# Optimization experiments

Hardware: AMD Instinct MI355X
Metric: run time of the kernel (lower is better)

The kernel has to match this reference:

```python
import jax, jax.numpy as jnp
import numpy as np

N_NODES = 50000
N_EDGES = 800000
D_FEAT = 128
DIM = 3
IN_CH = DIM + 2 * D_FEAT  # 259
HID = 256
OUT = 128


def setup_inputs() -> dict:
    key = jax.random.key(0)
    ks = jax.random.split(key, 10)
    x = jax.random.normal(ks[0], (N_NODES, D_FEAT), dtype=jnp.float32)
    pos = jax.random.normal(ks[1], (N_NODES, DIM), dtype=jnp.float32)
    edge_index = jax.random.randint(ks[2], (2, N_EDGES), 0, N_NODES, dtype=jnp.int64)
    s0 = 1.0 / np.sqrt(IN_CH)
    s2 = 1.0 / np.sqrt(HID)
    W0 = jax.random.uniform(ks[3], (HID, IN_CH), jnp.float32, -s0, s0)
    b0 = jax.random.uniform(ks[4], (HID,), jnp.float32, -s0, s0)
    W2 = jax.random.uniform(ks[5], (HID, HID), jnp.float32, -s2, s2)
    b2 = jax.random.uniform(ks[6], (HID,), jnp.float32, -s2, s2)
    W3 = jax.random.uniform(ks[7], (OUT, HID), jnp.float32, -s2, s2)
    b3 = jax.random.uniform(ks[8], (OUT,), jnp.float32, -s2, s2)
    return {"x": x, "edge_index": edge_index, "pos": pos,
            "W0": W0, "b0": b0, "W2": W2, "b2": b2, "W3": W3, "b3": b3}


def reference(x, edge_index, pos, W0, b0, W2, b2, W3, b3):
    src, dst = edge_index[0], edge_index[1]
    edge_attr = pos[dst] - pos[src]              # [E, 3]
    node_i = x[src]                              # [E, D]
    node_j = x[dst]                              # [E, D]
    inp = jnp.concatenate((edge_attr, node_i, node_j), axis=1)  # [E, 259]
    h = jax.nn.elu(inp @ W0.T + b0)
    h = jax.nn.elu(h @ W2.T + b2)
    return h @ W3.T + b3                         # [E, 128]
```

## Files before the change

kernel.cpp:

```cpp
#include <hip/hip_runtime.h>
#include <cstddef>
#include <cstdint>


#define N_NODES_C 50000
#define N_EDGES_C 800000
#define D_FEAT_C  128
#define IN_CH_C   259
#define HID_C     256
#define OUT_CH_C  128

#define BM6    64
#define HSTR6  264

typedef unsigned short u16;
typedef short bf16x8 __attribute__((ext_vector_type(8)));
typedef float f32x4 __attribute__((ext_vector_type(4)));

__device__ __forceinline__ u16 f2bf(float f) {
    union { float f; unsigned u; } v; v.f = f;
    unsigned u = v.u;
    return (u16)((u + 0x7fffu + ((u >> 16) & 1u)) >> 16);
}
__device__ __forceinline__ unsigned cvt_pk_bf16(float lo, float hi) {
    unsigned r;
    asm("v_cvt_pk_bf16_f32 %0, %1, %2" : "=v"(r) : "v"(lo), "v"(hi));
    return r;
}
__device__ __forceinline__ float bf2f_lo(unsigned u) {
    union { unsigned u; float f; } v; v.u = u << 16; return v.f;
}
__device__ __forceinline__ float bf2f_hi(unsigned u) {
    union { unsigned u; float f; } v; v.u = u & 0xFFFF0000u; return v.f;
}
__device__ __forceinline__ float elu1(float x) {
    return x > 0.0f ? x : (__expf(x) - 1.0f);
}
__device__ __forceinline__ unsigned addelu_pk(unsigned a, unsigned b) {
    float s0 = elu1(bf2f_lo(a) + bf2f_lo(b));
    float s1 = elu1(bf2f_hi(a) + bf2f_hi(b));
    return cvt_pk_bf16(s0, s1);
}

__global__ void detect_idx64(const void* __restrict__ ei_raw, int* __restrict__ flag) {
    if (blockIdx.x == 0 && threadIdx.x == 0) {
        const unsigned long long* p = (const unsigned long long*)ei_raw;
        int is64 = 1;
        for (int i = 0; i < 64; ++i)
            if (p[i] >= (1ULL << 32)) { is64 = 0; break; }
        *flag = is64;
    }
}

__global__ void prep_weights(const float* __restrict__ W0, const float* __restrict__ W2,
                             const float* __restrict__ W3, u16* __restrict__ WAB,
                             u16* __restrict__ W2f, u16* __restrict__ W3f) {
    int i = blockIdx.x * blockDim.x + threadIdx.x;
    const int nwab = 512 * 160, nw2 = 256 * 256, nw3 = 128 * 256;
    if (i < nwab) {
        int j = i / 160, k = i - j * 160;
        float v = 0.f;
        if (j < 256) {
            if (k < 128) v = W0[j * IN_CH_C + 3 + k];
            else if (k < 131) v = -W0[j * IN_CH_C + (k - 128)];
        } else {
            int j2 = j - 256;
            if (k < 128) v = W0[j2 * IN_CH_C + 131 + k];
            else if (k < 131) v = W0[j2 * IN_CH_C + (k - 128)];
        }
        WAB[i] = f2bf(v);
    } else if (i < nwab + nw2) {
        int q = i - nwab;
        int c = q & 7, lIdx = (q >> 3) & 63, kk = (q >> 9) & 7, jb = q >> 12;
        int j = jb * 16 + (lIdx & 15);
        int k = kk * 32 + ((lIdx >> 4) << 3) + c;
        W2f[q] = f2bf(W2[j * 256 + k]);
    } else if (i < nwab + nw2 + nw3) {
        int q = i - nwab - nw2;
        int c = q & 7, lIdx = (q >> 3) & 63, kk = (q >> 9) & 7, ob = q >> 12;
        int o = ob * 16 + (lIdx & 15);
        int k = kk * 32 + ((lIdx >> 4) << 3) + c;
        W3f[q] = f2bf(W3[o * 256 + k]);
    }
}

extern "C" __global__ void __launch_bounds__(512, 2)
node_gemm(const float* __restrict__ x, const float* __restrict__ pos,
          const u16* __restrict__ WAB, const float* __restrict__ b0,
          u16* __restrict__ AB) {
    __shared__ u16 tile[128 * 168];
    const int t = threadIdx.x;
    const int row0 = blockIdx.x * 128;
    for (int idx = t; idx < 128 * 80; idx += 512) {
        int m = idx / 80, wq = idx - m * 80;
        int k = wq * 2, n = row0 + m;
        float f0 = 0.f, f1 = 0.f;
        if (n < N_NODES_C) {
            f0 = (k < 128) ? x[(size_t)n * 128 + k] : (k < 131 ? pos[(size_t)n * 3 + k - 128] : 0.f);
            int k1 = k + 1;
            f1 = (k1 < 128) ? x[(size_t)n * 128 + k1] : (k1 < 131 ? pos[(size_t)n * 3 + k1 - 128] : 0.f);
        }
        *(unsigned*)&tile[m * 168 + k] = (unsigned)f2bf(f0) | ((unsigned)f2bf(f1) << 16);
    }
    __syncthreads();
    const int w = t >> 6, l = t & 63, lr = l & 15, hi = l >> 4;
    for (int mc = 0; mc < 2; ++mc) {
        f32x4 acc[4][4];
#pragma unroll
        for (int ji = 0; ji < 4; ++ji)
#pragma unroll
            for (int mi = 0; mi < 4; ++mi)
                acc[ji][mi] = (f32x4){0.f, 0.f, 0.f, 0.f};
#pragma unroll
        for (int kk = 0; kk < 5; ++kk) {
            bf16x8 af[4], bfr[4];
#pragma unroll
            for (int ji = 0; ji < 4; ++ji)
                af[ji] = *(const bf16x8*)&WAB[(size_t)(w * 64 + ji * 16 + lr) * 160 + kk * 32 + hi * 8];
#pragma unroll
            for (int mi = 0; mi < 4; ++mi)
                bfr[mi] = *(const bf16x8*)&tile[(mc * 64 + mi * 16 + lr) * 168 + kk * 32 + hi * 8];
#pragma unroll
            for (int ji = 0; ji < 4; ++ji)
#pragma unroll
                for (int mi = 0; mi < 4; ++mi)
                    acc[ji][mi] = __builtin_amdgcn_mfma_f32_16x16x32_bf16(af[ji], bfr[mi], acc[ji][mi], 0, 0, 0);
        }
#pragma unroll
        for (int ji = 0; ji < 4; ++ji) {
            int j0 = w * 64 + ji * 16 + hi * 4;
            float4 bb = make_float4(0.f, 0.f, 0.f, 0.f);
            if (j0 < 256) bb = *(const float4*)&b0[j0];
#pragma unroll
            for (int mi = 0; mi < 4; ++mi) {
                int nn = row0 + mc * 64 + mi * 16 + lr;
                if (nn < N_NODES_C) {
                    f32x4 v = acc[ji][mi];
                    uint2 pr;
                    pr.x = cvt_pk_bf16(v[0] + bb.x, v[1] + bb.y);
                    pr.y = cvt_pk_bf16(v[2] + bb.z, v[3] + bb.w);
                    *(uint2*)&AB[(size_t)nn * 512 + j0] = pr;
                }
            }
        }
    }
}

extern "C" __global__ void __launch_bounds__(256, 4)
edge_mlp_v6(const u16* __restrict__ AB, const void* __restrict__ ei_raw,
            const int* __restrict__ idx64_flag,
            const u16* __restrict__ W2f, const float* __restrict__ b2,
            const u16* __restrict__ W3f, const float* __restrict__ b3,
            float* __restrict__ out) {
    __shared__ u16 hbuf[BM6 * HSTR6];

    const int t = threadIdx.x;
    const int e0 = blockIdx.x * BM6;
    const int w = t >> 6, l = t & 63, lr = l & 15, hi = l >> 4;

    {
        const int m = t >> 2, q0 = (t & 3) * 2;
        const int eid = e0 + m;
        int sA, sB;
        if (*idx64_flag) {
            const long long* e = (const long long*)ei_raw;
            sA = (int)e[eid]; sB = (int)e[N_EDGES_C + eid];
        } else {
            const int* e = (const int*)ei_raw;
            sA = e[eid]; sB = e[N_EDGES_C + eid];
        }
        const u16* ra = AB + (size_t)sA * 512 + q0 * 32;
        const u16* rb = AB + (size_t)sB * 512 + 256 + q0 * 32;
        uint4 a[8], b[8];
#pragma unroll
        for (int i = 0; i < 8; ++i) a[i] = *(const uint4*)(ra + i * 8);
#pragma unroll
        for (int i = 0; i < 8; ++i) b[i] = *(const uint4*)(rb + i * 8);
#pragma unroll
        for (int i = 0; i < 8; ++i) {
            uint4 r;
            r.x = addelu_pk(a[i].x, b[i].x);
            r.y = addelu_pk(a[i].y, b[i].y);
            r.z = addelu_pk(a[i].z, b[i].z);
            r.w = addelu_pk(a[i].w, b[i].w);
            *(uint4*)&hbuf[m * HSTR6 + q0 * 32 + i * 8] = r;
        }
    }
    __syncthreads();

    f32x4 acc[4][4];
#pragma unroll
    for (int ji = 0; ji < 4; ++ji) {
        const float4 bb = *(const float4*)&b2[w * 64 + ji * 16 + hi * 4];
#pragma unroll
        for (int mi = 0; mi < 4; ++mi)
            acc[ji][mi] = (f32x4){bb.x, bb.y, bb.z, bb.w};
    }
    __builtin_amdgcn_s_setprio(1);
#pragma unroll
    for (int kk = 0; kk < 8; ++kk) {
        bf16x8 af[4], bfr[4];
#pragma unroll
        for (int ji = 0; ji < 4; ++ji)
            af[ji] = *(const bf16x8*)&W2f[(size_t)(((w * 4 + ji) * 8 + kk) * 64 + l) * 8];
#pragma unroll
        for (int mi = 0; mi < 4; ++mi)
            bfr[mi] = *(const bf16x8*)&hbuf[(mi * 16 + lr) * HSTR6 + kk * 32 + hi * 8];
#pragma unroll
        for (int ji = 0; ji < 4; ++ji)
#pragma unroll
            for (int mi = 0; mi < 4; ++mi)
                acc[ji][mi] = __builtin_amdgcn_mfma_f32_16x16x32_bf16(af[ji], bfr[mi], acc[ji][mi], 0, 0, 0);
    }
    __builtin_amdgcn_s_setprio(0);
    __syncthreads();

#pragma unroll
    for (int ji = 0; ji < 4; ++ji) {
        int j0 = w * 64 + ji * 16 + hi * 4;
#pragma unroll
        for (int mi = 0; mi < 4; ++mi) {
            int mm = mi * 16 + lr;
            f32x4 v = acc[ji][mi];
            uint2 pr;
            pr.x = cvt_pk_bf16(elu1(v[0]), elu1(v[1]));
            pr.y = cvt_pk_bf16(elu1(v[2]), elu1(v[3]));
            *(uint2*)&hbuf[mm * HSTR6 + j0] = pr;
        }
    }
    __syncthreads();

    f32x4 acc2[2][4];
#pragma unroll
    for (int oi = 0; oi < 2; ++oi) {
        const float4 bv = *(const float4*)&b3[w * 32 + oi * 16 + hi * 4];
#pragma unroll
        for (int mi = 0; mi < 4; ++mi)
            acc2[oi][mi] = (f32x4){bv.x, bv.y, bv.z, bv.w};
    }
    __builtin_amdgcn_s_setprio(1);
#pragma unroll
    for (int kk = 0; kk < 8; ++kk) {
        bf16x8 af3[2], bh[4];
#pragma unroll
        for (int oi = 0; oi < 2; ++oi)
            af3[oi] = *(const bf16x8*)&W3f[(size_t)(((w * 2 + oi) * 8 + kk) * 64 + l) * 8];
#pragma unroll
        for (int mi = 0; mi < 4; ++mi)
            bh[mi] = *(const bf16x8*)&hbuf[(mi * 16 + lr) * HSTR6 + kk * 32 + hi * 8];
#pragma unroll
        for (int oi = 0; oi < 2; ++oi)
#pragma unroll
            for (int mi = 0; mi < 4; ++mi)
                acc2[oi][mi] = __builtin_amdgcn_mfma_f32_16x16x32_bf16(af3[oi], bh[mi], acc2[oi][mi], 0, 0, 0);
    }
    __builtin_amdgcn_s_setprio(0);

#pragma unroll
    for (int oi = 0; oi < 2; ++oi)
#pragma unroll
        for (int mi = 0; mi < 4; ++mi) {
            f32x4 v = acc2[oi][mi];
            float4 o4;
            o4.x = v[0]; o4.y = v[1]; o4.z = v[2]; o4.w = v[3];
            *(float4*)&out[(size_t)(e0 + mi * 16 + lr) * 128
                           + w * 32 + oi * 16 + hi * 4] = o4;
        }
}

#define BM 64
#define PAD 65
__global__ void transpose_f32(const float* __restrict__ src, float* __restrict__ dst, int R, int C) {
    int i = blockIdx.x * blockDim.x + threadIdx.x;
    if (i < R * C) { int c = i / R; int r = i - c * R; dst[i] = src[r * C + c]; }
}
__device__ __forceinline__ void layer256(const float* __restrict__ wt, const float* __restrict__ b,
                                         const float* in_lds, float* out_lds, int K, int t) {
    const int jg = t & 63, mc = t >> 6;
    const float* wp = wt + jg * 4;
    const float4 bv = *(const float4*)&b[jg * 4];
    float acc[8][4];
#pragma unroll
    for (int i = 0; i < 8; ++i) { acc[i][0] = bv.x; acc[i][1] = bv.y; acc[i][2] = bv.z; acc[i][3] = bv.w; }
    const float* hbase = in_lds + mc * 8;
    float4 wv = *(const float4*)wp;
    for (int k = 0; k < K; ++k) {
        float4 wn = wv;
        if (k + 1 < K) wn = *(const float4*)(wp + (size_t)(k + 1) * HID_C);
        float h[8];
#pragma unroll
        for (int i = 0; i < 8; ++i) h[i] = hbase[k * PAD + i];
#pragma unroll
        for (int i = 0; i < 8; ++i) {
            acc[i][0] += h[i] * wv.x; acc[i][1] += h[i] * wv.y;
            acc[i][2] += h[i] * wv.z; acc[i][3] += h[i] * wv.w;
        }
        wv = wn;
    }
#pragma unroll
    for (int i4 = 0; i4 < 4; ++i4)
#pragma unroll
        for (int i = 0; i < 8; ++i) {
            float v = acc[i][i4];
            v = v > 0.0f ? v : expm1f(v);
            out_lds[(jg * 4 + i4) * PAD + mc * 8 + i] = v;
        }
}
extern "C" __global__ void __launch_bounds__(512, 2)
edge_mlp_f32(const float* __restrict__ x, const void* __restrict__ ei_raw,
             const float* __restrict__ pos, const int* __restrict__ idx64_flag,
             const float* __restrict__ wt0, const float* __restrict__ b0,
             const float* __restrict__ wt2, const float* __restrict__ b2,
             const float* __restrict__ wt3, const float* __restrict__ b3,
             float* __restrict__ out) {
    __shared__ float buf1[IN_CH_C * PAD];
    __shared__ float buf2[HID_C * PAD];
    __shared__ int s_src[BM], s_dst[BM];
    const int t = threadIdx.x;
    const int e0 = blockIdx.x * BM;
    if (t < BM) {
        int s, d;
        if (*idx64_flag) {
            const long long* e = (const long long*)ei_raw;
            s = (int)e[e0 + t]; d = (int)e[N_EDGES_C + e0 + t];
        } else {
            const int* e = (const int*)ei_raw;
            s = e[e0 + t]; d = e[N_EDGES_C + e0 + t];
        }
        s_src[t] = s; s_dst[t] = d;
    }
    __syncthreads();
    if (t < BM) {
        const int s = s_src[t], d = s_dst[t];
#pragma unroll
        for (int i = 0; i < 3; ++i)
            buf1[i * PAD + t] = pos[d * 3 + i] - pos[s * 3 + i];
    }
    {
        const int l = t & 31, grp = t >> 5;
#pragma unroll
        for (int r = 0; r < 4; ++r) {
            const int m = grp + r * 16;
            const int s = s_src[m], d = s_dst[m];
            const float4 xi = *(const float4*)&x[(size_t)s * D_FEAT_C + l * 4];
            const float4 xj = *(const float4*)&x[(size_t)d * D_FEAT_C + l * 4];
            buf1[(3 + l * 4 + 0) * PAD + m] = xi.x; buf1[(3 + l * 4 + 1) * PAD + m] = xi.y;
            buf1[(3 + l * 4 + 2) * PAD + m] = xi.z; buf1[(3 + l * 4 + 3) * PAD + m] = xi.w;
            buf1[(131 + l * 4 + 0) * PAD + m] = xj.x; buf1[(131 + l * 4 + 1) * PAD + m] = xj.y;
            buf1[(131 + l * 4 + 2) * PAD + m] = xj.z; buf1[(131 + l * 4 + 3) * PAD + m] = xj.w;
        }
    }
    __syncthreads();
    layer256(wt0, b0, buf1, buf2, IN_CH_C, t);
    __syncthreads();
    layer256(wt2, b2, buf2, buf1, HID_C, t);
    __syncthreads();
    {
        const int jg = t & 31, mc = t >> 5;
        const float* wp = wt3 + jg * 4;
        const float4 bv = *(const float4*)&b3[jg * 4];
        float acc[4][4];
#pragma unroll
        for (int i = 0; i < 4; ++i) { acc[i][0] = bv.x; acc[i][1] = bv.y; acc[i][2] = bv.z; acc[i][3] = bv.w; }
        const float* hbase = buf1 + mc * 4;
        float4 wv = *(const float4*)wp;
        for (int k = 0; k < HID_C; ++k) {
            float4 wn = wv;
            if (k + 1 < HID_C) wn = *(const float4*)(wp + (size_t)(k + 1) * OUT_CH_C);
            float h[4];
#pragma unroll
            for (int i = 0; i < 4; ++i) h[i] = hbase[k * PAD + i];
#pragma unroll
            for (int i = 0; i < 4; ++i) {
                acc[i][0] += h[i] * wv.x; acc[i][1] += h[i] * wv.y;
                acc[i][2] += h[i] * wv.z; acc[i][3] += h[i] * wv.w;
            }
            wv = wn;
        }
#pragma unroll
        for (int i = 0; i < 4; ++i) {
            float4 o;
            o.x = acc[i][0]; o.y = acc[i][1]; o.z = acc[i][2]; o.w = acc[i][3];
            *(float4*)&out[(size_t)(e0 + mc * 4 + i) * OUT_CH_C + jg * 4] = o;
        }
    }
}

extern "C" void kernel_launch(void* const* d_in, const int* in_sizes, int n_in,
                              void* d_out, int out_size, void* d_ws, size_t ws_size,
                              hipStream_t stream) {
    const float* x   = (const float*)d_in[0];
    const void*  ei  = d_in[1];
    const float* pos = (const float*)d_in[2];
    const float* W0  = (const float*)d_in[3];
    const float* b0  = (const float*)d_in[4];
    const float* W2  = (const float*)d_in[5];
    const float* b2  = (const float*)d_in[6];
    const float* W3  = (const float*)d_in[7];
    const float* b3  = (const float*)d_in[8];
    float* out = (float*)d_out;

    const size_t need = (size_t)N_NODES_C * 512 * 2 + (size_t)512 * 160 * 2
                      + (size_t)256 * 256 * 2 + (size_t)128 * 256 * 2 + 16;
    if (ws_size >= need) {
        u16* AB  = (u16*)d_ws;
        u16* WAB = AB + (size_t)N_NODES_C * 512;
        u16* W2f = WAB + 512 * 160;
        u16* W3f = W2f + 256 * 256;
        int* flag = (int*)(W3f + 128 * 256);

        detect_idx64<<<1, 64, 0, stream>>>(ei, flag);
        prep_weights<<<704, 256, 0, stream>>>(W0, W2, W3, WAB, W2f, W3f);
        node_gemm<<<391, 512, 0, stream>>>(x, pos, WAB, b0, AB);
        edge_mlp_v6<<<N_EDGES_C / BM6, 256, 0, stream>>>(AB, ei, flag, W2f, b2, W3f, b3, out);
    } else {
        float* wt0 = (float*)d_ws;
        float* wt2 = wt0 + IN_CH_C * HID_C;
        float* wt3 = wt2 + HID_C * HID_C;
        int*   flag = (int*)(wt3 + HID_C * OUT_CH_C);

        detect_idx64<<<1, 64, 0, stream>>>(ei, flag);
        int n0 = HID_C * IN_CH_C;
        transpose_f32<<<(n0 + 255) / 256, 256, 0, stream>>>(W0, wt0, HID_C, IN_CH_C);
        int n2 = HID_C * HID_C;
        transpose_f32<<<(n2 + 255) / 256, 256, 0, stream>>>(W2, wt2, HID_C, HID_C);
        int n3 = OUT_CH_C * HID_C;
        transpose_f32<<<(n3 + 255) / 256, 256, 0, stream>>>(W3, wt3, OUT_CH_C, HID_C);
        edge_mlp_f32<<<N_EDGES_C / BM, 512, 0, stream>>>(
            x, ei, pos, flag, wt0, b0, wt2, b2, wt3, b3, out);
    }
}
```

Measured before the change: 386.1 us.

## Make edge MLP kernel persistent with prefetched gathers and double LDS buffers

Replaces the one-tile-per-block edge MLP with a persistent kernel. A grid of 512 blocks with 512 threads each loops over edge tiles, and the gather of the next tile's node rows is issued before the current tile's GEMMs so that global latency overlaps compute. Two separate LDS buffers hold the layer-1 and layer-2 activations. Barriers wait only on LDS counters, which lets the in-flight global prefetch continue, and the work per wave is halved across eight waves. The trade-off is fewer resident waves per CU and more register pressure from holding the prefetched data across the loop.

```diff
diff --git a/kernel.cpp b/kernel.cpp
--- a/kernel.cpp
+++ b/kernel.cpp
@@ -10,8 +10,10 @@
 #define HID_C     256
 #define OUT_CH_C  128
 
-#define BM6    64
-#define HSTR6  264
+#define BM7    64
+#define NT7    (N_EDGES_C / BM7)
+#define GRID7  512
+#define HSTR7  264
 
 typedef unsigned short u16;
 typedef short bf16x8 __attribute__((ext_vector_type(8)));
@@ -40,6 +42,11 @@
     float s0 = elu1(bf2f_lo(a) + bf2f_lo(b));
     float s1 = elu1(bf2f_hi(a) + bf2f_hi(b));
     return cvt_pk_bf16(s0, s1);
+}
+__device__ __forceinline__ void barrier_lds_only() {
+    asm volatile("s_waitcnt lgkmcnt(0)" ::: "memory");
+    __builtin_amdgcn_s_barrier();
+    __builtin_amdgcn_sched_barrier(0);
 }
 
 __global__ void detect_idx64(const void* __restrict__ ei_raw, int* __restrict__ flag) {
@@ -146,126 +153,124 @@
     }
 }
 
-extern "C" __global__ void __launch_bounds__(256, 4)
-edge_mlp_v6(const u16* __restrict__ AB, const void* __restrict__ ei_raw,
+extern "C" __global__ void __launch_bounds__(512, 4)
+edge_mlp_v7(const u16* __restrict__ AB, const void* __restrict__ ei_raw,
             const int* __restrict__ idx64_flag,
             const u16* __restrict__ W2f, const float* __restrict__ b2,
             const u16* __restrict__ W3f, const float* __restrict__ b3,
             float* __restrict__ out) {
-    __shared__ u16 hbuf[BM6 * HSTR6];
+    __shared__ u16 h1[BM7 * HSTR7];
+    __shared__ u16 h2[BM7 * HSTR7];
 
     const int t = threadIdx.x;
-    const int e0 = blockIdx.x * BM6;
     const int w = t >> 6, l = t & 63, lr = l & 15, hi = l >> 4;
-
-    {
-        const int m = t >> 2, q0 = (t & 3) * 2;
-        const int eid = e0 + m;
-        int sA, sB;
-        if (*idx64_flag) {
-            const long long* e = (const long long*)ei_raw;
-            sA = (int)e[eid]; sB = (int)e[N_EDGES_C + eid];
-        } else {
-            const int* e = (const int*)ei_raw;
-            sA = e[eid]; sB = e[N_EDGES_C + eid];
-        }
-        const u16* ra = AB + (size_t)sA * 512 + q0 * 32;
-        const u16* rb = AB + (size_t)sB * 512 + 256 + q0 * 32;
-        uint4 a[8], b[8];
-#pragma unroll
-        for (int i = 0; i < 8; ++i) a[i] = *(const uint4*)(ra + i * 8);
-#pragma unroll
-        for (int i = 0; i < 8; ++i) b[i] = *(const uint4*)(rb + i * 8);
-#pragma unroll
-        for (int i = 0; i < 8; ++i) {
+    const int m = t >> 3, q = t & 7;
+    const int is64 = *idx64_flag;
+    const long long* e64 = (const long long*)ei_raw;
+    const int* e32 = (const int*)ei_raw;
+
+    float4 bb2[2];
+#pragma unroll
+    for (int ji = 0; ji < 2; ++ji)
+        bb2[ji] = *(const float4*)&b2[w * 32 + ji * 16 + hi * 4];
+    const float4 bb3 = *(const float4*)&b3[w * 16 + hi * 4];
+
+    uint4 ga[4], gb[4];
+#define GATHER(TL) do {                                                         \
+        int eid = (TL) * BM7 + m;                                               \
+        int sA, sB;                                                             \
+        if (is64) { sA = (int)e64[eid]; sB = (int)e64[N_EDGES_C + eid]; }       \
+        else      { sA = e32[eid];      sB = e32[N_EDGES_C + eid]; }            \
+        const u16* ra = AB + (size_t)sA * 512 + q * 32;                         \
+        const u16* rb = AB + (size_t)sB * 512 + 256 + q * 32;                   \
+        _Pragma("unroll")                                                       \
+        for (int i = 0; i < 4; ++i) { ga[i] = *(const uint4*)(ra + i * 8);      \
+                                      gb[i] = *(const uint4*)(rb + i * 8); }    \
+    } while (0)
+
+    const int tile0 = blockIdx.x;
+    GATHER(tile0);
+
+    for (int tk = tile0; tk < NT7; tk += GRID7) {
+#pragma unroll
+        for (int i = 0; i < 4; ++i) {
             uint4 r;
-            r.x = addelu_pk(a[i].x, b[i].x);
-            r.y = addelu_pk(a[i].y, b[i].y);
-            r.z = addelu_pk(a[i].z, b[i].z);
-            r.w = addelu_pk(a[i].w, b[i].w);
-            *(uint4*)&hbuf[m * HSTR6 + q0 * 32 + i * 8] = r;
-        }
-    }
-    __syncthreads();
-
-    f32x4 acc[4][4];
-#pragma unroll
-    for (int ji = 0; ji < 4; ++ji) {
-        const float4 bb = *(const float4*)&b2[w * 64 + ji * 16 + hi * 4];
+            r.x = addelu_pk(ga[i].x, gb[i].x);
+            r.y = addelu_pk(ga[i].y, gb[i].y);
+            r.z = addelu_pk(ga[i].z, gb[i].z);
+            r.w = addelu_pk(ga[i].w, gb[i].w);
+            *(uint4*)&h1[m * HSTR7 + q * 32 + i * 8] = r;
+        }
+        if (tk + GRID7 < NT7) GATHER(tk + GRID7);
+
+        barrier_lds_only();
+
+        f32x4 acc[2][4];
+#pragma unroll
+        for (int ji = 0; ji < 2; ++ji)
+#pragma unroll
+            for (int mi = 0; mi < 4; ++mi)
+                acc[ji][mi] = (f32x4){bb2[ji].x, bb2[ji].y, bb2[ji].z, bb2[ji].w};
+        __builtin_amdgcn_s_setprio(1);
+#pragma unroll
+        for (int kk = 0; kk < 8; ++kk) {
+            bf16x8 af[2], bfr[4];
+#pragma unroll
+            for (int ji = 0; ji < 2; ++ji)
+                af[ji] = *(const bf16x8*)&W2f[(size_t)(((w * 2 + ji) * 8 + kk) * 64 + l) * 8];
+#pragma unroll
+            for (int mi = 0; mi < 4; ++mi)
+                bfr[mi] = *(const bf16x8*)&h1[(mi * 16 + lr) * HSTR7 + kk * 32 + hi * 8];
+#pragma unroll
+            for (int ji = 0; ji < 2; ++ji)
+#pragma unroll
+                for (int mi = 0; mi < 4; ++mi)
+                    acc[ji][mi] = __builtin_amdgcn_mfma_f32_16x16x32_bf16(af[ji], bfr[mi], acc[ji][mi], 0, 0, 0);
+        }
+        __builtin_amdgcn_s_setprio(0);
+
+#pragma unroll
+        for (int ji = 0; ji < 2; ++ji) {
+            int j0 = w * 32 + ji * 16 + hi * 4;
+#pragma unroll
+            for (int mi = 0; mi < 4; ++mi) {
+                int mm = mi * 16 + lr;
+                f32x4 v = acc[ji][mi];
+                uint2 pr;
+                pr.x = cvt_pk_bf16(elu1(v[0]), elu1(v[1]));
+                pr.y = cvt_pk_bf16(elu1(v[2]), elu1(v[3]));
+                *(uint2*)&h2[mm * HSTR7 + j0] = pr;
+            }
+        }
+        barrier_lds_only();
+
+        f32x4 acc2[4];
 #pragma unroll
         for (int mi = 0; mi < 4; ++mi)
-            acc[ji][mi] = (f32x4){bb.x, bb.y, bb.z, bb.w};
-    }
-    __builtin_amdgcn_s_setprio(1);
-#pragma unroll
-    for (int kk = 0; kk < 8; ++kk) {
-        bf16x8 af[4], bfr[4];
-#pragma unroll
-        for (int ji = 0; ji < 4; ++ji)
-            af[ji] = *(const bf16x8*)&W2f[(size_t)(((w * 4 + ji) * 8 + kk) * 64 + l) * 8];
-#pragma unroll
-        for (int mi = 0; mi < 4; ++mi)
-            bfr[mi] = *(const bf16x8*)&hbuf[(mi * 16 + lr) * HSTR6 + kk * 32 + hi * 8];
-#pragma unroll
-        for (int ji = 0; ji < 4; ++ji)
-#pragma unroll
-            for (int mi = 0; mi < 4; ++mi)
-                acc[ji][mi] = __builtin_amdgcn_mfma_f32_16x16x32_bf16(af[ji], bfr[mi], acc[ji][mi], 0, 0, 0);
-    }
-    __builtin_amdgcn_s_setprio(0);
-    __syncthreads();
-
-#pragma unroll
-    for (int ji = 0; ji < 4; ++ji) {
-        int j0 = w * 64 + ji * 16 + hi * 4;
+            acc2[mi] = (f32x4){bb3.x, bb3.y, bb3.z, bb3.w};
+        __builtin_amdgcn_s_setprio(1);
+#pragma unroll
+        for (int kk = 0; kk < 8; ++kk) {
+            bf16x8 af3, bh[4];
+            af3 = *(const bf16x8*)&W3f[(size_t)((w * 8 + kk) * 64 + l) * 8];
+#pragma unroll
+            for (int mi = 0; mi < 4; ++mi)
+                bh[mi] = *(const bf16x8*)&h2[(mi * 16 + lr) * HSTR7 + kk * 32 + hi * 8];
+#pragma unroll
+            for (int mi = 0; mi < 4; ++mi)
+                acc2[mi] = __builtin_amdgcn_mfma_f32_16x16x32_bf16(af3, bh[mi], acc2[mi], 0, 0, 0);
+        }
+        __builtin_amdgcn_s_setprio(0);
+
 #pragma unroll
         for (int mi = 0; mi < 4; ++mi) {
-            int mm = mi * 16 + lr;
-            f32x4 v = acc[ji][mi];
-            uint2 pr;
-            pr.x = cvt_pk_bf16(elu1(v[0]), elu1(v[1]));
-            pr.y = cvt_pk_bf16(elu1(v[2]), elu1(v[3]));
-            *(uint2*)&hbuf[mm * HSTR6 + j0] = pr;
-        }
-    }
-    __syncthreads();
-
-    f32x4 acc2[2][4];
-#pragma unroll
-    for (int oi = 0; oi < 2; ++oi) {
-        const float4 bv = *(const float4*)&b3[w * 32 + oi * 16 + hi * 4];
-#pragma unroll
-        for (int mi = 0; mi < 4; ++mi)
-            acc2[oi][mi] = (f32x4){bv.x, bv.y, bv.z, bv.w};
-    }
-    __builtin_amdgcn_s_setprio(1);
-#pragma unroll
-    for (int kk = 0; kk < 8; ++kk) {
-        bf16x8 af3[2], bh[4];
-#pragma unroll
-        for (int oi = 0; oi < 2; ++oi)
-            af3[oi] = *(const bf16x8*)&W3f[(size_t)(((w * 2 + oi) * 8 + kk) * 64 + l) * 8];
-#pragma unroll
-        for (int mi = 0; mi < 4; ++mi)
-            bh[mi] = *(const bf16x8*)&hbuf[(mi * 16 + lr) * HSTR6 + kk * 32 + hi * 8];
-#pragma unroll
-        for (int oi = 0; oi < 2; ++oi)
-#pragma unroll
-            for (int mi = 0; mi < 4; ++mi)
-                acc2[oi][mi] = __builtin_amdgcn_mfma_f32_16x16x32_bf16(af3[oi], bh[mi], acc2[oi][mi], 0, 0, 0);
-    }
-    __builtin_amdgcn_s_setprio(0);
-
-#pragma unroll
-    for (int oi = 0; oi < 2; ++oi)
-#pragma unroll
-        for (int mi = 0; mi < 4; ++mi) {
-            f32x4 v = acc2[oi][mi];
+            f32x4 v = acc2[mi];
             float4 o4;
             o4.x = v[0]; o4.y = v[1]; o4.z = v[2]; o4.w = v[3];
-            *(float4*)&out[(size_t)(e0 + mi * 16 + lr) * 128
-                           + w * 32 + oi * 16 + hi * 4] = o4;
-        }
+            *(float4*)&out[(size_t)(tk * BM7 + mi * 16 + lr) * 128 + w * 16 + hi * 4] = o4;
+        }
+    }
+#undef GATHER
 }
 
 #define BM 64
@@ -412,7 +417,7 @@
         detect_idx64<<<1, 64, 0, stream>>>(ei, flag);
         prep_weights<<<704, 256, 0, stream>>>(W0, W2, W3, WAB, W2f, W3f);
         node_gemm<<<391, 512, 0, stream>>>(x, pos, WAB, b0, AB);
-        edge_mlp_v6<<<N_EDGES_C / BM6, 256, 0, stream>>>(AB, ei, flag, W2f, b2, W3f, b3, out);
+        edge_mlp_v7<<<GRID7, 512, 0, stream>>>(AB, ei, flag, W2f, b2, W3f, b3, out);
     } else {
         float* wt0 = (float*)d_ws;
         float* wt2 = wt0 + IN_CH_C * HID_C;
```

Result: slower. 511.2 us (+32.4%).

## Split edge MLP over eight waves with swizzled double LDS buffers

Applied to the files above, without the earlier changes.

The edge MLP kernel moves from 256 to 512 threads per 64-edge block. Each wave now computes half as many output columns, so there are more waves to hide latency and fewer accumulators per wave. The gather is spread across more threads, and separate h1/h2 LDS buffers remove one barrier. An XOR swizzle on the LDS columns is meant to reduce bank conflicts, at the cost of doubled shared memory per block, which may limit occupancy.

```diff
diff --git a/kernel.cpp b/kernel.cpp
--- a/kernel.cpp
+++ b/kernel.cpp
@@ -10,8 +10,9 @@
 #define HID_C     256
 #define OUT_CH_C  128
 
-#define BM6    64
-#define HSTR6  264
+#define BM8    64
+#define HSTR8  272
+#define SW(row, c) ((c) ^ (((row) & 7) << 3))
 
 typedef unsigned short u16;
 typedef short bf16x8 __attribute__((ext_vector_type(8)));
@@ -146,20 +147,21 @@
     }
 }
 
-extern "C" __global__ void __launch_bounds__(256, 4)
-edge_mlp_v6(const u16* __restrict__ AB, const void* __restrict__ ei_raw,
+extern "C" __global__ void __launch_bounds__(512, 4)
+edge_mlp_v8(const u16* __restrict__ AB, const void* __restrict__ ei_raw,
             const int* __restrict__ idx64_flag,
             const u16* __restrict__ W2f, const float* __restrict__ b2,
             const u16* __restrict__ W3f, const float* __restrict__ b3,
             float* __restrict__ out) {
-    __shared__ u16 hbuf[BM6 * HSTR6];
+    __shared__ u16 h1[BM8 * HSTR8];
+    __shared__ u16 h2[BM8 * HSTR8];
 
     const int t = threadIdx.x;
-    const int e0 = blockIdx.x * BM6;
+    const int e0 = blockIdx.x * BM8;
     const int w = t >> 6, l = t & 63, lr = l & 15, hi = l >> 4;
 
     {
-        const int m = t >> 2, q0 = (t & 3) * 2;
+        const int m = t >> 3, q = t & 7;
         const int eid = e0 + m;
         int sA, sB;
         if (*idx64_flag) {
@@ -169,29 +171,29 @@
             const int* e = (const int*)ei_raw;
             sA = e[eid]; sB = e[N_EDGES_C + eid];
         }
-        const u16* ra = AB + (size_t)sA * 512 + q0 * 32;
-        const u16* rb = AB + (size_t)sB * 512 + 256 + q0 * 32;
-        uint4 a[8], b[8];
-#pragma unroll
-        for (int i = 0; i < 8; ++i) a[i] = *(const uint4*)(ra + i * 8);
-#pragma unroll
-        for (int i = 0; i < 8; ++i) b[i] = *(const uint4*)(rb + i * 8);
-#pragma unroll
-        for (int i = 0; i < 8; ++i) {
+        const u16* ra = AB + (size_t)sA * 512 + q * 32;
+        const u16* rb = AB + (size_t)sB * 512 + 256 + q * 32;
+        uint4 a[4], b[4];
+#pragma unroll
+        for (int i = 0; i < 4; ++i) a[i] = *(const uint4*)(ra + i * 8);
+#pragma unroll
+        for (int i = 0; i < 4; ++i) b[i] = *(const uint4*)(rb + i * 8);
+#pragma unroll
+        for (int i = 0; i < 4; ++i) {
             uint4 r;
             r.x = addelu_pk(a[i].x, b[i].x);
             r.y = addelu_pk(a[i].y, b[i].y);
             r.z = addelu_pk(a[i].z, b[i].z);
             r.w = addelu_pk(a[i].w, b[i].w);
-            *(uint4*)&hbuf[m * HSTR6 + q0 * 32 + i * 8] = r;
-        }
-    }
-    __syncthreads();
-
-    f32x4 acc[4][4];
-#pragma unroll
-    for (int ji = 0; ji < 4; ++ji) {
-        const float4 bb = *(const float4*)&b2[w * 64 + ji * 16 + hi * 4];
+            *(uint4*)&h1[m * HSTR8 + SW(m, q * 32 + i * 8)] = r;
+        }
+    }
+    __syncthreads();
+
+    f32x4 acc[2][4];
+#pragma unroll
+    for (int ji = 0; ji < 2; ++ji) {
+        const float4 bb = *(const float4*)&b2[w * 32 + ji * 16 + hi * 4];
 #pragma unroll
         for (int mi = 0; mi < 4; ++mi)
             acc[ji][mi] = (f32x4){bb.x, bb.y, bb.z, bb.w};
@@ -199,25 +201,26 @@
     __builtin_amdgcn_s_setprio(1);
 #pragma unroll
     for (int kk = 0; kk < 8; ++kk) {
-        bf16x8 af[4], bfr[4];
-#pragma unroll
-        for (int ji = 0; ji < 4; ++ji)
-            af[ji] = *(const bf16x8*)&W2f[(size_t)(((w * 4 + ji) * 8 + kk) * 64 + l) * 8];
-#pragma unroll
-        for (int mi = 0; mi < 4; ++mi)
-            bfr[mi] = *(const bf16x8*)&hbuf[(mi * 16 + lr) * HSTR6 + kk * 32 + hi * 8];
-#pragma unroll
-        for (int ji = 0; ji < 4; ++ji)
+        bf16x8 af[2], bfr[4];
+#pragma unroll
+        for (int ji = 0; ji < 2; ++ji)
+            af[ji] = *(const bf16x8*)&W2f[(size_t)(((w * 2 + ji) * 8 + kk) * 64 + l) * 8];
+#pragma unroll
+        for (int mi = 0; mi < 4; ++mi) {
+            int row = mi * 16 + lr;
+            bfr[mi] = *(const bf16x8*)&h1[row * HSTR8 + SW(row, kk * 32 + hi * 8)];
+        }
+#pragma unroll
+        for (int ji = 0; ji < 2; ++ji)
 #pragma unroll
             for (int mi = 0; mi < 4; ++mi)
                 acc[ji][mi] = __builtin_amdgcn_mfma_f32_16x16x32_bf16(af[ji], bfr[mi], acc[ji][mi], 0, 0, 0);
     }
     __builtin_amdgcn_s_setprio(0);
-    __syncthreads();
-
-#pragma unroll
-    for (int ji = 0; ji < 4; ++ji) {
-        int j0 = w * 64 + ji * 16 + hi * 4;
+
+#pragma unroll
+    for (int ji = 0; ji < 2; ++ji) {
+        int j0 = w * 32 + ji * 16 + hi * 4;
 #pragma unroll
         for (int mi = 0; mi < 4; ++mi) {
             int mm = mi * 16 + lr;
@@ -225,47 +228,41 @@
             uint2 pr;
             pr.x = cvt_pk_bf16(elu1(v[0]), elu1(v[1]));
             pr.y = cvt_pk_bf16(elu1(v[2]), elu1(v[3]));
-            *(uint2*)&hbuf[mm * HSTR6 + j0] = pr;
-        }
-    }
-    __syncthreads();
-
-    f32x4 acc2[2][4];
-#pragma unroll
-    for (int oi = 0; oi < 2; ++oi) {
-        const float4 bv = *(const float4*)&b3[w * 32 + oi * 16 + hi * 4];
+            *(uint2*)&h2[mm * HSTR8 + SW(mm, j0)] = pr;
+        }
+    }
+    __syncthreads();
+
+    f32x4 acc2[4];
+    {
+        const float4 bv = *(const float4*)&b3[w * 16 + hi * 4];
 #pragma unroll
         for (int mi = 0; mi < 4; ++mi)
-            acc2[oi][mi] = (f32x4){bv.x, bv.y, bv.z, bv.w};
+            acc2[mi] = (f32x4){bv.x, bv.y, bv.z, bv.w};
     }
     __builtin_amdgcn_s_setprio(1);
 #pragma unroll
     for (int kk = 0; kk < 8; ++kk) {
-        bf16x8 af3[2], bh[4];
-#pragma unroll
-        for (int oi = 0; oi < 2; ++oi)
-            af3[oi] = *(const bf16x8*)&W3f[(size_t)(((w * 2 + oi) * 8 + kk) * 64 + l) * 8];
+        bf16x8 af3, bh[4];
+        af3 = *(const bf16x8*)&W3f[(size_t)((w * 8 + kk) * 64 + l) * 8];
+#pragma unroll
+        for (int mi = 0; mi < 4; ++mi) {
+            int row = mi * 16 + lr;
+            bh[mi] = *(const bf16x8*)&h2[row * HSTR8 + SW(row, kk * 32 + hi * 8)];
+        }
 #pragma unroll
         for (int mi = 0; mi < 4; ++mi)
-            bh[mi] = *(const bf16x8*)&hbuf[(mi * 16 + lr) * HSTR6 + kk * 32 + hi * 8];
-#pragma unroll
-        for (int oi = 0; oi < 2; ++oi)
-#pragma unroll
-            for (int mi = 0; mi < 4; ++mi)
-                acc2[oi][mi] = __builtin_amdgcn_mfma_f32_16x16x32_bf16(af3[oi], bh[mi], acc2[oi][mi], 0, 0, 0);
+            acc2[mi] = __builtin_amdgcn_mfma_f32_16x16x32_bf16(af3, bh[mi], acc2[mi], 0, 0, 0);
     }
     __builtin_amdgcn_s_setprio(0);
 
 #pragma unroll
-    for (int oi = 0; oi < 2; ++oi)
-#pragma unroll
-        for (int mi = 0; mi < 4; ++mi) {
-            f32x4 v = acc2[oi][mi];
-            float4 o4;
-            o4.x = v[0]; o4.y = v[1]; o4.z = v[2]; o4.w = v[3];
-            *(float4*)&out[(size_t)(e0 + mi * 16 + lr) * 128
-                           + w * 32 + oi * 16 + hi * 4] = o4;
-        }
+    for (int mi = 0; mi < 4; ++mi) {
+        f32x4 v = acc2[mi];
+        float4 o4;
+        o4.x = v[0]; o4.y = v[1]; o4.z = v[2]; o4.w = v[3];
+        *(float4*)&out[(size_t)(e0 + mi * 16 + lr) * 128 + w * 16 + hi * 4] = o4;
+    }
 }
 
 #define BM 64
@@ -412,7 +409,7 @@
         detect_idx64<<<1, 64, 0, stream>>>(ei, flag);
         prep_weights<<<704, 256, 0, stream>>>(W0, W2, W3, WAB, W2f, W3f);
         node_gemm<<<391, 512, 0, stream>>>(x, pos, WAB, b0, AB);
-        edge_mlp_v6<<<N_EDGES_C / BM6, 256, 0, stream>>>(AB, ei, flag, W2f, b2, W3f, b3, out);
+        edge_mlp_v8<<<N_EDGES_C / BM8, 512, 0, stream>>>(AB, ei, flag, W2f, b2, W3f, b3, out);
     } else {
         float* wt0 = (float*)d_ws;
         float* wt2 = wt0 + IN_CH_C * HID_C;
```

Result: faster. 369.7 us (-4.2%).
